# Kernel tuning notes

Hardware: AMD Instinct MI355X
Metric: run time of the kernel (lower is better)

## Reference

```python
import jax, jax.numpy as jnp
import numpy as np

S, B, H = 512, 64, 1024


def setup_inputs() -> dict:
    key = jax.random.key(0)
    ks = jax.random.split(key, 9)
    sc = 1.0 / np.sqrt(2 * H)
    return {
        "hidden": jax.random.normal(ks[0], (B, H), jnp.float32),
        "decoder_out": jax.random.normal(ks[1], (B, H), jnp.float32),
        "encoder_states": jax.random.normal(ks[2], (S, B, H), jnp.float32),
        "W_attn": jax.random.uniform(ks[3], (2 * H, 2 * H), jnp.float32, -sc, sc),
        "b_attn": jax.random.uniform(ks[4], (2 * H,), jnp.float32, -sc, sc),
        "W_attn2": jax.random.uniform(ks[5], (1, 2 * H), jnp.float32, -sc, sc),
        "b_attn2": jax.random.uniform(ks[6], (1,), jnp.float32, -sc, sc),
        "W_comb": jax.random.uniform(ks[7], (H, 2 * H), jnp.float32, -sc, sc),
        "b_comb": jax.random.uniform(ks[8], (H,), jnp.float32, -sc, sc),
    }


def reference(hidden, decoder_out, encoder_states, W_attn, b_attn, W_attn2, b_attn2, W_comb, b_comb):
    s, b, h = encoder_states.shape
    # per-timestep cat(hidden, enc_t) -> attn -> tanh -> attn2, fully batched over S
    hid = jnp.broadcast_to(hidden[None], (s, b, h))
    cat = jnp.concatenate([hid, encoder_states], axis=-1)            # [S,B,2H]
    scores = jnp.tanh(cat @ W_attn.T + b_attn) @ W_attn2.T + b_attn2  # [S,B,1]
    scores = scores[..., 0].T                                         # [B,S] (stack dim=1 + squeeze)
    attn_w = jax.nn.softmax(scores, axis=-1)                          # [B,S]
    # bmm([B,1,S], [B,S,H]) -> [B,H]
    applied = jnp.einsum("bs,sbh->bh", attn_w, encoder_states)
    out = jnp.concatenate([decoder_out, applied], axis=-1) @ W_comb.T + b_comb
    out = jnp.tanh(out)
    return out, applied
```

## Files before the change

kernel.cpp:

```cpp
#include <hip/hip_runtime.h>
#include <stdint.h>


typedef __attribute__((ext_vector_type(8))) short bf16x8;
typedef __attribute__((ext_vector_type(4))) float f32x4;

__device__ __forceinline__ float bf2f(uint16_t u) {
  return __uint_as_float(((uint32_t)u) << 16);
}
__device__ __forceinline__ uint16_t f2bf(float x) {
  uint32_t u = __float_as_uint(x);
  u += 0x7fffu + ((u >> 16) & 1u);
  return (uint16_t)(u >> 16);
}
__device__ __forceinline__ uint32_t pk2(float a, float b) {
  return (uint32_t)f2bf(a) | ((uint32_t)f2bf(b) << 16);
}
__device__ __forceinline__ uint4 cvt8(const float* __restrict__ p) {
  const float4 a = *(const float4*)p;
  const float4 b = *(const float4*)(p + 4);
  uint4 r;
  r.x = pk2(a.x, a.y); r.y = pk2(a.z, a.w);
  r.z = pk2(b.x, b.y); r.w = pk2(b.z, b.w);
  return r;
}
__device__ __forceinline__ float tanh_fast(float x) {
  const float e = __expf(2.f * x);
  return __builtin_fmaf(-2.f, __builtin_amdgcn_rcpf(e + 1.f), 1.f);
}
__device__ __forceinline__ void load16(const uint16_t* g, uint16_t* l) {
  __builtin_amdgcn_global_load_lds(
      (const __attribute__((address_space(1))) void*)g,
      (__attribute__((address_space(3))) void*)l, 16, 0, 0);
}

__global__ __launch_bounds__(256)
void init_kernel(float* __restrict__ scores, float* __restrict__ U,
                 const float* __restrict__ ba) {
  const int tid = blockIdx.x * 256 + threadIdx.x;
  scores[tid] = 0.f;
#pragma unroll
  for (int k = 0; k < 4; ++k) {
    const int i = tid * 4 + k;
    U[i] = ba[i & 2047];
  }
}

__global__ __launch_bounds__(256)
void cvt_all_kernel(const float* __restrict__ enc, const float* __restrict__ Wa,
                    const float* __restrict__ Wc,
                    uint16_t* __restrict__ enc_bf, uint16_t* __restrict__ Wa_bf,
                    uint16_t* __restrict__ Wc_bf) {
  const int stride = gridDim.x * 256;
  for (int idx = blockIdx.x * 256 + threadIdx.x; idx < 4718592; idx += stride) {
    if (idx < 4194304) {
      ((uint4*)enc_bf)[idx] = cvt8(enc + (size_t)idx * 8);
    } else if (idx < 4456448) {
      const int k = idx - 4194304;
      const int j = k >> 7, c8 = k & 127;
      ((uint4*)Wa_bf)[k] = cvt8(Wa + (size_t)j * 2048 + 1024 + c8 * 8);
    } else {
      const int k = idx - 4456448;
      ((uint4*)Wc_bf)[k] = cvt8(Wc + (size_t)k * 8);
    }
  }
}

__global__ __launch_bounds__(256)
void gemm_u_kernel(const float* __restrict__ A, const float* __restrict__ B32,
                   float* __restrict__ U) {
  __shared__ __align__(16) uint16_t sA[128 * 32];
  __shared__ __align__(16) uint16_t sB[128 * 32];
  const int t = threadIdx.x, lane = t & 63, wave = t >> 6;
  const int wm = wave >> 1, wn = wave & 1;
  const int bn0 = blockIdx.x * 128;
  const int kbase = blockIdx.y * 256;
  const int srow = t >> 2, scol = (t & 3) * 8;
  const int ar0 = min(srow, 63), ar1 = min(64 + srow, 63);
  f32x4 acc[4][4];
#pragma unroll
  for (int i = 0; i < 4; ++i)
#pragma unroll
    for (int j = 0; j < 4; ++j) acc[i][j] = (f32x4){0.f, 0.f, 0.f, 0.f};
  const int mrow = wm * 64 + (lane & 15);
  const int nrow = wn * 64 + (lane & 15);
  const int kq = (lane >> 4) * 8;
  for (int kk = 0; kk < 8; ++kk) {
    const int k0 = kbase + (kk << 5);
    const uint4 va0 = cvt8(A + (size_t)ar0 * 1024 + scol + k0);
    const uint4 va1 = cvt8(A + (size_t)ar1 * 1024 + scol + k0);
    const uint4 vb0 = cvt8(B32 + (size_t)(bn0 + srow) * 2048 + scol + k0);
    const uint4 vb1 = cvt8(B32 + (size_t)(bn0 + 64 + srow) * 2048 + scol + k0);
    __syncthreads();
    *(uint4*)&sA[t * 8] = va0;
    *(uint4*)&sA[2048 + t * 8] = va1;
    *(uint4*)&sB[t * 8] = vb0;
    *(uint4*)&sB[2048 + t * 8] = vb1;
    __syncthreads();
    bf16x8 af[4], bfr[4];
#pragma unroll
    for (int i = 0; i < 4; ++i) af[i] = *(const bf16x8*)&sA[(mrow + i * 16) * 32 + kq];
#pragma unroll
    for (int j = 0; j < 4; ++j) bfr[j] = *(const bf16x8*)&sB[(nrow + j * 16) * 32 + kq];
#pragma unroll
    for (int i = 0; i < 4; ++i)
#pragma unroll
      for (int j = 0; j < 4; ++j)
        acc[i][j] = __builtin_amdgcn_mfma_f32_16x16x32_bf16(af[i], bfr[j], acc[i][j], 0, 0, 0);
  }
  const int colb = lane & 15, rquad = lane >> 4;
#pragma unroll
  for (int i = 0; i < 4; ++i)
#pragma unroll
    for (int r = 0; r < 4; ++r) {
      const int gm = wm * 64 + i * 16 + rquad * 4 + r;
      if (gm < 64) {
#pragma unroll
        for (int j = 0; j < 4; ++j) {
          const int gn = bn0 + wn * 64 + j * 16 + colb;
          atomicAdd(&U[gm * 2048 + gn], acc[i][j][r]);
        }
      }
    }
}

template <int MODE>
__global__ __launch_bounds__(256)
void gemm_bf_kernel(const uint16_t* __restrict__ A, int lda,
                    const uint16_t* __restrict__ Bm, int ldb,
                    int M, int K,
                    float* __restrict__ outf,
                    const float* __restrict__ Ubias,
                    const float* __restrict__ bias) {
  __shared__ __align__(16) uint16_t sAB[2][2][4096];
  float* sU = (float*)sAB;

  const int t = threadIdx.x, lane = t & 63, wave = t >> 6;
  const int wm = wave >> 1, wn = wave & 1;
  const int bm0 = blockIdx.x * 128;
  const int bn0 = blockIdx.y * 128;
  const int kbase = (MODE == 3) ? (int)blockIdx.z * 512 : 0;
  const int nsteps = ((MODE == 3) ? 512 : K) >> 5;

  const int srow = t >> 2, scol = (t & 3) * 8;
  const int ar0 = min(bm0 + srow, M - 1);
  const int ar1 = min(bm0 + 64 + srow, M - 1);
  const uint16_t* agp0 = A + (size_t)ar0 * lda + scol + kbase;
  const uint16_t* agp1 = A + (size_t)ar1 * lda + scol + kbase;
  const uint16_t* bgp0 = Bm + (size_t)(bn0 + srow) * ldb + scol + kbase;
  const uint16_t* bgp1 = Bm + (size_t)(bn0 + 64 + srow) * ldb + scol + kbase;
  const int so = wave * 512;

  f32x4 acc[4][4];
#pragma unroll
  for (int i = 0; i < 4; ++i)
#pragma unroll
    for (int j = 0; j < 4; ++j) acc[i][j] = (f32x4){0.f, 0.f, 0.f, 0.f};

  const int mrow = wm * 64 + (lane & 15);
  const int nrow = wn * 64 + (lane & 15);
  const int kq = (lane >> 4) * 8;

  load16(agp0, &sAB[0][0][so]);
  load16(agp1, &sAB[0][0][2048 + so]);
  load16(bgp0, &sAB[0][1][so]);
  load16(bgp1, &sAB[0][1][2048 + so]);
  __syncthreads();

  int cur = 0;
  for (int kk = 0; kk < nsteps - 1; ++kk) {
    const int k0 = (kk + 1) << 5;
    load16(agp0 + k0, &sAB[cur ^ 1][0][so]);
    load16(agp1 + k0, &sAB[cur ^ 1][0][2048 + so]);
    load16(bgp0 + k0, &sAB[cur ^ 1][1][so]);
    load16(bgp1 + k0, &sAB[cur ^ 1][1][2048 + so]);

    const uint16_t* sA = sAB[cur][0];
    const uint16_t* sB = sAB[cur][1];
    bf16x8 af[4], bfr[4];
#pragma unroll
    for (int i = 0; i < 4; ++i) af[i] = *(const bf16x8*)&sA[(mrow + i * 16) * 32 + kq];
#pragma unroll
    for (int j = 0; j < 4; ++j) bfr[j] = *(const bf16x8*)&sB[(nrow + j * 16) * 32 + kq];
#pragma unroll
    for (int i = 0; i < 4; ++i)
#pragma unroll
      for (int j = 0; j < 4; ++j)
        acc[i][j] = __builtin_amdgcn_mfma_f32_16x16x32_bf16(af[i], bfr[j], acc[i][j], 0, 0, 0);
    __syncthreads();
    cur ^= 1;
  }
  {
    const uint16_t* sA = sAB[cur][0];
    const uint16_t* sB = sAB[cur][1];
    bf16x8 af[4], bfr[4];
#pragma unroll
    for (int i = 0; i < 4; ++i) af[i] = *(const bf16x8*)&sA[(mrow + i * 16) * 32 + kq];
#pragma unroll
    for (int j = 0; j < 4; ++j) bfr[j] = *(const bf16x8*)&sB[(nrow + j * 16) * 32 + kq];
#pragma unroll
    for (int i = 0; i < 4; ++i)
#pragma unroll
      for (int j = 0; j < 4; ++j)
        acc[i][j] = __builtin_amdgcn_mfma_f32_16x16x32_bf16(af[i], bfr[j], acc[i][j], 0, 0, 0);
    __syncthreads();
  }

  const int colb = lane & 15, rquad = lane >> 4;
  if (MODE == 1) {
#pragma unroll
    for (int q = 0; q < 8; ++q) {
      const int idx = t + q * 256;
      const int b = idx >> 5, c4 = idx & 31;
      ((float4*)sU)[idx] = *(const float4*)&Ubias[b * 2048 + bn0 + c4 * 4];
    }
    __syncthreads();
    float w2f[4];
#pragma unroll
    for (int j = 0; j < 4; ++j) w2f[j] = bias[bn0 + wn * 64 + j * 16 + colb];
#pragma unroll
    for (int i = 0; i < 4; ++i) {
#pragma unroll
      for (int r = 0; r < 4; ++r) {
        const int gm = bm0 + wm * 64 + i * 16 + rquad * 4 + r;
        const int bb = gm & 63;
        float p = 0.f;
#pragma unroll
        for (int j = 0; j < 4; ++j) {
          const float u = sU[bb * 128 + wn * 64 + j * 16 + colb];
          p += tanh_fast(acc[i][j][r] + u) * w2f[j];
        }
        p += __shfl_xor(p, 1);
        p += __shfl_xor(p, 2);
        p += __shfl_xor(p, 4);
        p += __shfl_xor(p, 8);
        if (colb == 0) atomicAdd(outf + gm, p);
      }
    }
  } else if (MODE == 2) {
#pragma unroll
    for (int i = 0; i < 4; ++i)
#pragma unroll
      for (int r = 0; r < 4; ++r) {
        const int gm = bm0 + wm * 64 + i * 16 + rquad * 4 + r;
        if (gm < M) {
#pragma unroll
          for (int j = 0; j < 4; ++j) {
            const int gn = bn0 + wn * 64 + j * 16 + colb;
            outf[gm * 1024 + gn] = tanh_fast(acc[i][j][r] + bias[gn]);
          }
        }
      }
  } else {
    const float bsc = (blockIdx.z == 0) ? 1.f : 0.f;
#pragma unroll
    for (int i = 0; i < 4; ++i)
#pragma unroll
      for (int r = 0; r < 4; ++r) {
        const int gm = bm0 + wm * 64 + i * 16 + rquad * 4 + r;
        if (gm < M) {
#pragma unroll
          for (int j = 0; j < 4; ++j) {
            const int gn = bn0 + wn * 64 + j * 16 + colb;
            atomicAdd(outf + gm * 1024 + gn, acc[i][j][r] + bsc * bias[gn]);
          }
        }
      }
  }
}

__global__ __launch_bounds__(256)
void applied_kernel(const uint16_t* __restrict__ encb, const float* __restrict__ dec,
                    const float* __restrict__ scores,
                    float* __restrict__ out_applied, uint16_t* __restrict__ acat,
                    float* __restrict__ out_acc) {
  const int b = blockIdx.x, chunk = blockIdx.y, t = threadIdx.x;
  const int wave = t >> 6, lane = t & 63;
  __shared__ float w[512];
  __shared__ float red[8];
  __shared__ float2 part2[256];
  float v0 = scores[(size_t)t * 64 + b];
  float v1 = scores[(size_t)(t + 256) * 64 + b];
  float mx = fmaxf(v0, v1);
#pragma unroll
  for (int off = 32; off >= 1; off >>= 1) mx = fmaxf(mx, __shfl_xor(mx, off));
  if (lane == 0) red[wave] = mx;
  __syncthreads();
  mx = fmaxf(fmaxf(red[0], red[1]), fmaxf(red[2], red[3]));
  const float e0 = __expf(v0 - mx), e1 = __expf(v1 - mx);
  float sum = e0 + e1;
#pragma unroll
  for (int off = 32; off >= 1; off >>= 1) sum += __shfl_xor(sum, off);
  if (lane == 0) red[4 + wave] = sum;
  __syncthreads();
  sum = (red[4] + red[5]) + (red[6] + red[7]);
  const float inv = 1.f / sum;
  w[t] = e0 * inv;
  w[t + 256] = e1 * inv;
  __syncthreads();
  const int hp = t & 31, sq = t >> 5;
  const int h = chunk * 64 + hp * 2;
  const uint32_t* base = (const uint32_t*)encb + (size_t)b * 512 + (h >> 1);
  float a0 = 0.f, a1 = 0.f;
#pragma unroll 8
  for (int s = sq * 64; s < sq * 64 + 64; ++s) {
    const uint32_t p = base[(size_t)s * 32768];
    a0 += w[s] * bf2f((uint16_t)(p & 0xffffu));
    a1 += w[s] * bf2f((uint16_t)(p >> 16));
  }
  part2[t] = make_float2(a0, a1);
  __syncthreads();
  if (t < 32) {
    a0 = 0.f; a1 = 0.f;
#pragma unroll
    for (int k = 0; k < 8; ++k) {
      const float2 pp = part2[t + 32 * k];
      a0 += pp.x; a1 += pp.y;
    }
    *(float2*)(out_applied + (size_t)b * 1024 + h) = make_float2(a0, a1);
    *(uint32_t*)(acat + (size_t)b * 2048 + 1024 + h) = pk2(a0, a1);
    *(uint32_t*)(acat + (size_t)b * 2048 + h) =
        pk2(dec[(size_t)b * 1024 + h], dec[(size_t)b * 1024 + h + 1]);
    *(float2*)(out_acc + (size_t)b * 1024 + h) = make_float2(0.f, 0.f);
  }
}

__global__ __launch_bounds__(256)
void tanh_kernel(const float* __restrict__ acc, float* __restrict__ outp) {
  const int i = blockIdx.x * 256 + threadIdx.x;
  float4 v = ((const float4*)acc)[i];
  v.x = tanh_fast(v.x); v.y = tanh_fast(v.y);
  v.z = tanh_fast(v.z); v.w = tanh_fast(v.w);
  ((float4*)outp)[i] = v;
}

extern "C" void kernel_launch(void* const* d_in, const int* in_sizes, int n_in,
                              void* d_out, int out_size, void* d_ws, size_t ws_size,
                              hipStream_t stream) {
  const float* hidden  = (const float*)d_in[0];
  const float* dec     = (const float*)d_in[1];
  const float* enc     = (const float*)d_in[2];
  const float* W_attn  = (const float*)d_in[3];
  const float* b_attn  = (const float*)d_in[4];
  const float* W_attn2 = (const float*)d_in[5];
  const float* W_comb  = (const float*)d_in[7];
  const float* b_comb  = (const float*)d_in[8];
  float* outp = (float*)d_out;

  char* ws = (char*)d_ws;
  float*    scores = (float*)(ws + 0);
  float*    U      = (float*)(ws + 131072);
  float*    out_acc= (float*)(ws + 131072);
  uint16_t* acat   = (uint16_t*)(ws + 655360);
  uint16_t* enc_bf = (uint16_t*)(ws + 1048576);
  uint16_t* Wa_bf  = (uint16_t*)(ws + 68157440);
  uint16_t* Wc_bf  = (uint16_t*)(ws + 72351744);

  init_kernel<<<128, 256, 0, stream>>>(scores, U, b_attn);
  cvt_all_kernel<<<4608, 256, 0, stream>>>(enc, W_attn, W_comb, enc_bf, Wa_bf, Wc_bf);
  gemm_u_kernel<<<dim3(16, 4), 256, 0, stream>>>(hidden, W_attn, U);
  gemm_bf_kernel<1><<<dim3(256, 16), 256, 0, stream>>>(
      enc_bf, 1024, Wa_bf, 1024, 32768, 1024, scores, U, W_attn2);
  applied_kernel<<<dim3(64, 16), 256, 0, stream>>>(enc_bf, dec, scores,
                                                   outp + 65536, acat, out_acc);
  gemm_bf_kernel<3><<<dim3(1, 8, 4), 256, 0, stream>>>(
      acat, 2048, Wc_bf, 2048, 64, 2048, out_acc, nullptr, b_comb);
  tanh_kernel<<<64, 256, 0, stream>>>(out_acc, outp);
}
```

Before: 475.4 us.

## Triple-buffer bf16 GEMM LDS pipeline with XOR swizzle and vmcnt waits

Replaces the double-buffered LDS pipeline in the bf16 MFMA GEMM with a three-stage ring. The next-next tile is prefetched while the current one is consumed, and synchronisation uses a partial vmcnt wait plus a bare s_barrier instead of a full __syncthreads. LDS chunks are XOR-swizzled per row to cut bank conflicts on the bf16x8 fragment reads. The MODE 1 epilogue now reads Ubias straight from global memory instead of staging it in LDS. The unused MODE 2 epilogue is removed, and LDS use grows to three buffers.

```diff
diff --git a/kernel.cpp b/kernel.cpp
--- a/kernel.cpp
+++ b/kernel.cpp
@@ -132,24 +132,27 @@
                     float* __restrict__ outf,
                     const float* __restrict__ Ubias,
                     const float* __restrict__ bias) {
-  __shared__ __align__(16) uint16_t sAB[2][2][4096];
-  float* sU = (float*)sAB;
+  __shared__ __align__(16) uint16_t lds[3][2][4096];
 
   const int t = threadIdx.x, lane = t & 63, wave = t >> 6;
   const int wm = wave >> 1, wn = wave & 1;
   const int bm0 = blockIdx.x * 128;
   const int bn0 = blockIdx.y * 128;
   const int kbase = (MODE == 3) ? (int)blockIdx.z * 512 : 0;
-  const int nsteps = ((MODE == 3) ? 512 : K) >> 5;
-
-  const int srow = t >> 2, scol = (t & 3) * 8;
-  const int ar0 = min(bm0 + srow, M - 1);
-  const int ar1 = min(bm0 + 64 + srow, M - 1);
-  const uint16_t* agp0 = A + (size_t)ar0 * lda + scol + kbase;
-  const uint16_t* agp1 = A + (size_t)ar1 * lda + scol + kbase;
-  const uint16_t* bgp0 = Bm + (size_t)(bn0 + srow) * ldb + scol + kbase;
-  const uint16_t* bgp1 = Bm + (size_t)(bn0 + 64 + srow) * ldb + scol + kbase;
-  const int so = wave * 512;
+  const int nt = ((MODE == 3) ? 512 : K) >> 5;
+
+  const uint16_t* gpA[2];
+  const uint16_t* gpB[2];
+  int sb[2];
+#pragma unroll
+  for (int q = 0; q < 2; ++q) {
+    const int s = q * 256 + t;
+    const int r = s >> 2, kc = s & 3;
+    const int g = kc ^ ((r >> 1) & 3);
+    gpA[q] = A + (size_t)min(bm0 + r, M - 1) * lda + kbase + g * 8;
+    gpB[q] = Bm + (size_t)(bn0 + r) * ldb + kbase + g * 8;
+    sb[q] = (q * 256 + wave * 64) * 8;
+  }
 
   f32x4 acc[4][4];
 #pragma unroll
@@ -157,64 +160,53 @@
 #pragma unroll
     for (int j = 0; j < 4; ++j) acc[i][j] = (f32x4){0.f, 0.f, 0.f, 0.f};
 
-  const int mrow = wm * 64 + (lane & 15);
-  const int nrow = wn * 64 + (lane & 15);
-  const int kq = (lane >> 4) * 8;
-
-  load16(agp0, &sAB[0][0][so]);
-  load16(agp1, &sAB[0][0][2048 + so]);
-  load16(bgp0, &sAB[0][1][so]);
-  load16(bgp1, &sAB[0][1][2048 + so]);
-  __syncthreads();
-
-  int cur = 0;
-  for (int kk = 0; kk < nsteps - 1; ++kk) {
-    const int k0 = (kk + 1) << 5;
-    load16(agp0 + k0, &sAB[cur ^ 1][0][so]);
-    load16(agp1 + k0, &sAB[cur ^ 1][0][2048 + so]);
-    load16(bgp0 + k0, &sAB[cur ^ 1][1][so]);
-    load16(bgp1 + k0, &sAB[cur ^ 1][1][2048 + so]);
-
-    const uint16_t* sA = sAB[cur][0];
-    const uint16_t* sB = sAB[cur][1];
+  const int swz = ((lane >> 1) & 3) << 3;
+  const int kq = ((lane >> 4) * 8) ^ swz;
+  const int aoff = (wm * 64 + (lane & 15)) * 32 + kq;
+  const int boff = (wn * 64 + (lane & 15)) * 32 + kq;
+
+#pragma unroll
+  for (int q = 0; q < 2; ++q) {
+    load16(gpA[q], &lds[0][0][sb[q]]);
+    load16(gpB[q], &lds[0][1][sb[q]]);
+  }
+#pragma unroll
+  for (int q = 0; q < 2; ++q) {
+    load16(gpA[q] + 32, &lds[1][0][sb[q]]);
+    load16(gpB[q] + 32, &lds[1][1][sb[q]]);
+  }
+  asm volatile("s_waitcnt vmcnt(4)" ::: "memory");
+  __builtin_amdgcn_s_barrier();
+
+  int cur = 0, nx2 = 2;
+  for (int kt = 0; kt < nt; ++kt) {
+    const int kpre = (kt + 2 < nt) ? (kt + 2) * 32 : (nt - 1) * 32;
+#pragma unroll
+    for (int q = 0; q < 2; ++q) {
+      load16(gpA[q] + kpre, &lds[nx2][0][sb[q]]);
+      load16(gpB[q] + kpre, &lds[nx2][1][sb[q]]);
+    }
+    const uint16_t* sA = lds[cur][0];
+    const uint16_t* sB = lds[cur][1];
     bf16x8 af[4], bfr[4];
 #pragma unroll
-    for (int i = 0; i < 4; ++i) af[i] = *(const bf16x8*)&sA[(mrow + i * 16) * 32 + kq];
-#pragma unroll
-    for (int j = 0; j < 4; ++j) bfr[j] = *(const bf16x8*)&sB[(nrow + j * 16) * 32 + kq];
+    for (int i = 0; i < 4; ++i) af[i] = *(const bf16x8*)&sA[aoff + i * 512];
+#pragma unroll
+    for (int j = 0; j < 4; ++j) bfr[j] = *(const bf16x8*)&sB[boff + j * 512];
 #pragma unroll
     for (int i = 0; i < 4; ++i)
 #pragma unroll
       for (int j = 0; j < 4; ++j)
         acc[i][j] = __builtin_amdgcn_mfma_f32_16x16x32_bf16(af[i], bfr[j], acc[i][j], 0, 0, 0);
-    __syncthreads();
-    cur ^= 1;
-  }
-  {
-    const uint16_t* sA = sAB[cur][0];
-    const uint16_t* sB = sAB[cur][1];
-    bf16x8 af[4], bfr[4];
-#pragma unroll
-    for (int i = 0; i < 4; ++i) af[i] = *(const bf16x8*)&sA[(mrow + i * 16) * 32 + kq];
-#pragma unroll
-    for (int j = 0; j < 4; ++j) bfr[j] = *(const bf16x8*)&sB[(nrow + j * 16) * 32 + kq];
-#pragma unroll
-    for (int i = 0; i < 4; ++i)
-#pragma unroll
-      for (int j = 0; j < 4; ++j)
-        acc[i][j] = __builtin_amdgcn_mfma_f32_16x16x32_bf16(af[i], bfr[j], acc[i][j], 0, 0, 0);
-    __syncthreads();
-  }
+    asm volatile("s_waitcnt vmcnt(4)" ::: "memory");
+    __builtin_amdgcn_s_barrier();
+    cur = (cur == 2) ? 0 : cur + 1;
+    nx2 = (nx2 == 2) ? 0 : nx2 + 1;
+  }
+  asm volatile("s_waitcnt vmcnt(0)" ::: "memory");
 
   const int colb = lane & 15, rquad = lane >> 4;
   if (MODE == 1) {
-#pragma unroll
-    for (int q = 0; q < 8; ++q) {
-      const int idx = t + q * 256;
-      const int b = idx >> 5, c4 = idx & 31;
-      ((float4*)sU)[idx] = *(const float4*)&Ubias[b * 2048 + bn0 + c4 * 4];
-    }
-    __syncthreads();
     float w2f[4];
 #pragma unroll
     for (int j = 0; j < 4; ++j) w2f[j] = bias[bn0 + wn * 64 + j * 16 + colb];
@@ -227,7 +219,7 @@
         float p = 0.f;
 #pragma unroll
         for (int j = 0; j < 4; ++j) {
-          const float u = sU[bb * 128 + wn * 64 + j * 16 + colb];
+          const float u = Ubias[bb * 2048 + bn0 + wn * 64 + j * 16 + colb];
           p += tanh_fast(acc[i][j][r] + u) * w2f[j];
         }
         p += __shfl_xor(p, 1);
@@ -237,20 +229,6 @@
         if (colb == 0) atomicAdd(outf + gm, p);
       }
     }
-  } else if (MODE == 2) {
-#pragma unroll
-    for (int i = 0; i < 4; ++i)
-#pragma unroll
-      for (int r = 0; r < 4; ++r) {
-        const int gm = bm0 + wm * 64 + i * 16 + rquad * 4 + r;
-        if (gm < M) {
-#pragma unroll
-          for (int j = 0; j < 4; ++j) {
-            const int gn = bn0 + wn * 64 + j * 16 + colb;
-            outf[gm * 1024 + gn] = tanh_fast(acc[i][j][r] + bias[gn]);
-          }
-        }
-      }
   } else {
     const float bsc = (blockIdx.z == 0) ? 1.f : 0.f;
 #pragma unroll
```

Result: no change. 484.8 us (+2.0%).
